# Performance work log

Hardware: AMD Instinct MI355X
Metric: run time of the kernel (lower is better)

Reference implementation:

```python
import jax, jax.numpy as jnp
import numpy as np

N, E, D, C = 40000, 640000, 128, 64


def setup_inputs() -> dict:
    key = jax.random.key(0)
    ks = jax.random.split(key, 12)
    x = jax.random.normal(ks[0], (N, D), dtype=jnp.float32)
    edge_row = jax.random.randint(ks[1], (E,), 0, N, dtype=jnp.int32)
    edge_col = jax.random.randint(ks[2], (E,), 0, N, dtype=jnp.int32)
    edge_val = jax.random.uniform(ks[3], (E,), dtype=jnp.float32)
    s1 = 1.0 / np.sqrt(D)
    W1 = jax.random.uniform(ks[4], (D, D), minval=-s1, maxval=s1, dtype=jnp.float32)
    b1 = jax.random.uniform(ks[5], (D,), minval=-s1, maxval=s1, dtype=jnp.float32)
    W2 = jax.random.uniform(ks[6], (D, D), minval=-s1, maxval=s1, dtype=jnp.float32)
    b2 = jax.random.uniform(ks[7], (D,), minval=-s1, maxval=s1, dtype=jnp.float32)
    Wf = jax.random.uniform(ks[8], (D, C), minval=-s1, maxval=s1, dtype=jnp.float32)
    bf = jax.random.uniform(ks[9], (C,), minval=-s1, maxval=s1, dtype=jnp.float32)
    return {"x": x, "edge_row": edge_row, "edge_col": edge_col, "edge_val": edge_val,
            "W1": W1, "b1": b1, "W2": W2, "b2": b2, "Wf": Wf, "bf": bf}


def _spmm(row, col, val, dense):
    # out[row] += val * dense[col]  == adj @ dense with adj in COO form
    msgs = dense[col] * val[:, None]  # [E, D]
    return jax.ops.segment_sum(msgs, row, num_segments=N)


def reference(x, edge_row, edge_col, edge_val, W1, b1, W2, b2, Wf, bf):
    # gc1: relu(adj @ (x @ W1) + b1)
    h = jax.nn.relu(_spmm(edge_row, edge_col, edge_val, x @ W1) + b1)
    # dropout(p=0.2, training=False) -> identity in eval mode
    # gc2 + residual: relu(adj @ (h @ W2) + b2) + h
    h2 = jax.nn.relu(_spmm(edge_row, edge_col, edge_val, h @ W2) + b2) + h
    # final linear classifier
    return h2 @ Wf + bf
```

## Files before the change

kernel.cpp:

```cpp
#include <hip/hip_runtime.h>

#define N_NODES 40000
#define N_EDGES 640000
#define DIM     128
#define NCLS    64
#define CAP     64
#define CSTRIDE 16

typedef __attribute__((ext_vector_type(8))) short short8v;
typedef __attribute__((ext_vector_type(4))) float f32x4;

__device__ __forceinline__ unsigned short f2bf(float f) {
    unsigned int u = __float_as_uint(f);
    unsigned int r = u + 0x7fffu + ((u >> 16) & 1u);
    return (unsigned short)(r >> 16);
}
__device__ __forceinline__ float bf2f(unsigned int s) {
    return __uint_as_float(s << 16);
}
__device__ __forceinline__ float4 dec4(uint2 u) {
    return make_float4(bf2f(u.x & 0xffffu), bf2f(u.x >> 16),
                       bf2f(u.y & 0xffffu), bf2f(u.y >> 16));
}

__launch_bounds__(256)
__global__ void prep(const float* __restrict__ W1, const float* __restrict__ W2,
                     const float* __restrict__ Wf,
                     unsigned short* __restrict__ wt1, unsigned short* __restrict__ wt2,
                     unsigned short* __restrict__ wtf, int* __restrict__ counts) {
    const int b = blockIdx.x, tid = threadIdx.x;
    if (b < 2500) {
        counts[b * 256 + tid] = 0;
    } else if (b < 2564) {
        int e = (b - 2500) * 256 + tid;
        int k = e >> 7, n = e & 127;
        wt1[n * 128 + k] = f2bf(W1[e]);
    } else if (b < 2628) {
        int e = (b - 2564) * 256 + tid;
        int k = e >> 7, n = e & 127;
        wt2[n * 128 + k] = f2bf(W2[e]);
    } else {
        int e = (b - 2628) * 256 + tid;
        int k = e >> 6, n = e & 63;
        wtf[n * 128 + k] = f2bf(Wf[e]);
    }
}

__launch_bounds__(256)
__global__ void build_bucket(const int* __restrict__ erow, const int* __restrict__ ecol,
                             const float* __restrict__ evalv, int* __restrict__ counts,
                             uint2* __restrict__ bslot) {
    int e = blockIdx.x * blockDim.x + threadIdx.x;
    if (e >= N_EDGES) return;
    int r = erow[e];
    int p = atomicAdd(&counts[r * CSTRIDE], 1);
    if (p < CAP)
        bslot[(size_t)r * CAP + p] = make_uint2((unsigned)ecol[e], __float_as_uint(evalv[e]));
}

__launch_bounds__(256)
__global__ void gemm_f32A_bf16(const float* __restrict__ A,
                               const unsigned short* __restrict__ WT,
                               unsigned short* __restrict__ C) {
    __shared__ unsigned short sB[128 * 128];
    const int tid = threadIdx.x;
    for (int c = tid; c < 2048; c += 256) {
        int n = c >> 4, j = c & 15;
        short8v v = *reinterpret_cast<const short8v*>(WT + n * 128 + 8 * j);
        *reinterpret_cast<short8v*>(&sB[n * 128 + 8 * (j ^ (n & 7))]) = v;
    }
    __syncthreads();

    const int lane = tid & 63;
    const int wv   = tid >> 6;
    const int m0   = blockIdx.x * 64 + wv * 16;
    const int r    = lane & 15;
    const int g    = lane >> 4;

    short8v af[4];
    const float* arow = A + (size_t)(m0 + r) * 128 + 8 * g;
#pragma unroll
    for (int f = 0; f < 4; ++f) {
        float4 p = *reinterpret_cast<const float4*>(arow + 32 * f);
        float4 q = *reinterpret_cast<const float4*>(arow + 32 * f + 4);
        short8v a;
        a[0] = (short)f2bf(p.x); a[1] = (short)f2bf(p.y);
        a[2] = (short)f2bf(p.z); a[3] = (short)f2bf(p.w);
        a[4] = (short)f2bf(q.x); a[5] = (short)f2bf(q.y);
        a[6] = (short)f2bf(q.z); a[7] = (short)f2bf(q.w);
        af[f] = a;
    }

    f32x4 acc[8];
#pragma unroll
    for (int nt = 0; nt < 8; ++nt) acc[nt] = (f32x4){0.f, 0.f, 0.f, 0.f};

#pragma unroll
    for (int nt = 0; nt < 8; ++nt) {
        const int rw = nt * 16 + r;
        const unsigned short* bbase = &sB[rw * 128];
#pragma unroll
        for (int f = 0; f < 4; ++f) {
            short8v bfr = *reinterpret_cast<const short8v*>(bbase + 8 * ((4 * f + g) ^ (rw & 7)));
            acc[nt] = __builtin_amdgcn_mfma_f32_16x16x32_bf16(af[f], bfr, acc[nt], 0, 0, 0);
        }
    }
#pragma unroll
    for (int nt = 0; nt < 8; ++nt)
#pragma unroll
        for (int rr = 0; rr < 4; ++rr)
            C[(size_t)(m0 + g * 4 + rr) * 128 + nt * 16 + r] = f2bf(acc[nt][rr]);
}

__launch_bounds__(256)
__global__ void gemm_bf16_128(const unsigned short* __restrict__ A,
                              const unsigned short* __restrict__ WT,
                              unsigned short* __restrict__ C) {
    __shared__ unsigned short sB[128 * 128];
    const int tid = threadIdx.x;
    for (int c = tid; c < 2048; c += 256) {
        int n = c >> 4, j = c & 15;
        short8v v = *reinterpret_cast<const short8v*>(WT + n * 128 + 8 * j);
        *reinterpret_cast<short8v*>(&sB[n * 128 + 8 * (j ^ (n & 7))]) = v;
    }
    __syncthreads();

    const int lane = tid & 63;
    const int wv   = tid >> 6;
    const int m0   = blockIdx.x * 64 + wv * 16;
    const int r    = lane & 15;
    const int g    = lane >> 4;

    short8v af[4];
    const unsigned short* arow = A + (size_t)(m0 + r) * 128 + 8 * g;
#pragma unroll
    for (int f = 0; f < 4; ++f)
        af[f] = *reinterpret_cast<const short8v*>(arow + 32 * f);

    f32x4 acc[8];
#pragma unroll
    for (int nt = 0; nt < 8; ++nt) acc[nt] = (f32x4){0.f, 0.f, 0.f, 0.f};

#pragma unroll
    for (int nt = 0; nt < 8; ++nt) {
        const int rw = nt * 16 + r;
        const unsigned short* bbase = &sB[rw * 128];
#pragma unroll
        for (int f = 0; f < 4; ++f) {
            short8v bfr = *reinterpret_cast<const short8v*>(bbase + 8 * ((4 * f + g) ^ (rw & 7)));
            acc[nt] = __builtin_amdgcn_mfma_f32_16x16x32_bf16(af[f], bfr, acc[nt], 0, 0, 0);
        }
    }
#pragma unroll
    for (int nt = 0; nt < 8; ++nt)
#pragma unroll
        for (int rr = 0; rr < 4; ++rr)
            C[(size_t)(m0 + g * 4 + rr) * 128 + nt * 16 + r] = f2bf(acc[nt][rr]);
}

__launch_bounds__(256)
__global__ void gemm_bf16_final(const unsigned short* __restrict__ A,
                                const unsigned short* __restrict__ WT,
                                const float* __restrict__ bias,
                                float* __restrict__ C) {
    __shared__ unsigned short sB[64 * 128];
    const int tid = threadIdx.x;
    for (int c = tid; c < 1024; c += 256) {
        int n = c >> 4, j = c & 15;
        short8v v = *reinterpret_cast<const short8v*>(WT + n * 128 + 8 * j);
        *reinterpret_cast<short8v*>(&sB[n * 128 + 8 * (j ^ (n & 7))]) = v;
    }
    __syncthreads();

    const int lane = tid & 63;
    const int wv   = tid >> 6;
    const int m0   = blockIdx.x * 64 + wv * 16;
    const int r    = lane & 15;
    const int g    = lane >> 4;

    short8v af[4];
    const unsigned short* arow = A + (size_t)(m0 + r) * 128 + 8 * g;
#pragma unroll
    for (int f = 0; f < 4; ++f)
        af[f] = *reinterpret_cast<const short8v*>(arow + 32 * f);

    f32x4 acc[4];
#pragma unroll
    for (int nt = 0; nt < 4; ++nt) acc[nt] = (f32x4){0.f, 0.f, 0.f, 0.f};

#pragma unroll
    for (int nt = 0; nt < 4; ++nt) {
        const int rw = nt * 16 + r;
        const unsigned short* bbase = &sB[rw * 128];
#pragma unroll
        for (int f = 0; f < 4; ++f) {
            short8v bfr = *reinterpret_cast<const short8v*>(bbase + 8 * ((4 * f + g) ^ (rw & 7)));
            acc[nt] = __builtin_amdgcn_mfma_f32_16x16x32_bf16(af[f], bfr, acc[nt], 0, 0, 0);
        }
    }
#pragma unroll
    for (int nt = 0; nt < 4; ++nt)
#pragma unroll
        for (int rr = 0; rr < 4; ++rr)
            C[(size_t)(m0 + g * 4 + rr) * 64 + nt * 16 + r] = acc[nt][rr] + bias[nt * 16 + r];
}

__launch_bounds__(256)
__global__ void spmm_fused_bf16(const uint2* __restrict__ dense2,
                                const uint2* __restrict__ bslot,
                                const int* __restrict__ counts,
                                const float4* __restrict__ bias4,
                                const uint2* __restrict__ residbf,
                                uint2* __restrict__ outbf) {
    const int lane = threadIdx.x & 63;
    const int half = lane >> 5;
    const int sub  = lane & 31;
    const int row  = blockIdx.x * 4 + (threadIdx.x >> 6);
    int deg = counts[row * CSTRIDE];
    if (deg > CAP) deg = CAP;

    int   colr = 0;
    float valr = 0.f;
    if (lane < deg) {
        uint2 s = bslot[(size_t)row * CAP + lane];
        colr = (int)s.x;
        valr = __uint_as_float(s.y);
    }
    const int degUp = (deg + 7) & ~7;

    float ax0 = 0.f, ay0 = 0.f, az0 = 0.f, aw0 = 0.f;
    float ax1 = 0.f, ay1 = 0.f, az1 = 0.f, aw1 = 0.f;
    float ax2 = 0.f, ay2 = 0.f, az2 = 0.f, aw2 = 0.f;
    float ax3 = 0.f, ay3 = 0.f, az3 = 0.f, aw3 = 0.f;
    for (int i = 0; i < degUp; i += 8) {
        int   c0 = __shfl(colr, i + 0 + half); float v0 = __shfl(valr, i + 0 + half);
        int   c1 = __shfl(colr, i + 2 + half); float v1 = __shfl(valr, i + 2 + half);
        int   c2 = __shfl(colr, i + 4 + half); float v2 = __shfl(valr, i + 4 + half);
        int   c3 = __shfl(colr, i + 6 + half); float v3 = __shfl(valr, i + 6 + half);
        uint2 u0 = dense2[(size_t)c0 * 32 + sub];
        uint2 u1 = dense2[(size_t)c1 * 32 + sub];
        uint2 u2 = dense2[(size_t)c2 * 32 + sub];
        uint2 u3 = dense2[(size_t)c3 * 32 + sub];
        float4 d0 = dec4(u0); ax0 += v0 * d0.x; ay0 += v0 * d0.y; az0 += v0 * d0.z; aw0 += v0 * d0.w;
        float4 d1 = dec4(u1); ax1 += v1 * d1.x; ay1 += v1 * d1.y; az1 += v1 * d1.z; aw1 += v1 * d1.w;
        float4 d2 = dec4(u2); ax2 += v2 * d2.x; ay2 += v2 * d2.y; az2 += v2 * d2.z; aw2 += v2 * d2.w;
        float4 d3 = dec4(u3); ax3 += v3 * d3.x; ay3 += v3 * d3.y; az3 += v3 * d3.z; aw3 += v3 * d3.w;
    }
    float sx = (ax0 + ax1) + (ax2 + ax3);
    float sy = (ay0 + ay1) + (ay2 + ay3);
    float sz = (az0 + az1) + (az2 + az3);
    float sw = (aw0 + aw1) + (aw2 + aw3);
    sx += __shfl_xor(sx, 32);
    sy += __shfl_xor(sy, 32);
    sz += __shfl_xor(sz, 32);
    sw += __shfl_xor(sw, 32);

    if (half == 0) {
        float4 bb = bias4[sub];
        sx = fmaxf(sx + bb.x, 0.f);
        sy = fmaxf(sy + bb.y, 0.f);
        sz = fmaxf(sz + bb.z, 0.f);
        sw = fmaxf(sw + bb.w, 0.f);
        if (residbf) {
            float4 rr = dec4(residbf[(size_t)row * 32 + sub]);
            sx += rr.x; sy += rr.y; sz += rr.z; sw += rr.w;
        }
        outbf[(size_t)row * 32 + sub] =
            make_uint2((unsigned)f2bf(sx) | ((unsigned)f2bf(sy) << 16),
                       (unsigned)f2bf(sz) | ((unsigned)f2bf(sw) << 16));
    }
}

extern "C" void kernel_launch(void* const* d_in, const int* in_sizes, int n_in,
                              void* d_out, int out_size, void* d_ws, size_t ws_size,
                              hipStream_t stream) {
    const float* x    = (const float*)d_in[0];
    const int*   erow = (const int*)  d_in[1];
    const int*   ecol = (const int*)  d_in[2];
    const float* ev   = (const float*)d_in[3];
    const float* W1   = (const float*)d_in[4];
    const float* b1   = (const float*)d_in[5];
    const float* W2   = (const float*)d_in[6];
    const float* b2   = (const float*)d_in[7];
    const float* Wf   = (const float*)d_in[8];
    const float* bf   = (const float*)d_in[9];
    float* out = (float*)d_out;

    const size_t MB = 1u << 20;
    char* ws = (char*)d_ws;
    int*            counts = (int*)           (ws + 0 * MB);
    uint2*          bslot  = (uint2*)         (ws + 4 * MB);
    unsigned short* gb     = (unsigned short*)(ws + 25 * MB);
    unsigned short* hb     = (unsigned short*)(ws + 36 * MB);
    unsigned short* h2b    = (unsigned short*)(ws + 47 * MB);
    unsigned short* wt1    = (unsigned short*)(ws + 58 * MB);
    unsigned short* wt2    = (unsigned short*)(ws + 58 * MB + 65536);
    unsigned short* wtf    = (unsigned short*)(ws + 58 * MB + 131072);

    prep<<<2660, 256, 0, stream>>>(W1, W2, Wf, wt1, wt2, wtf, counts);
    build_bucket<<<(N_EDGES + 255) / 256, 256, 0, stream>>>(erow, ecol, ev, counts, bslot);

    gemm_f32A_bf16<<<N_NODES / 64, 256, 0, stream>>>(x, wt1, gb);
    spmm_fused_bf16<<<N_NODES / 4, 256, 0, stream>>>((const uint2*)gb, bslot, counts,
                                                     (const float4*)b1, nullptr,
                                                     (uint2*)hb);
    gemm_bf16_128<<<N_NODES / 64, 256, 0, stream>>>(hb, wt2, gb);
    spmm_fused_bf16<<<N_NODES / 4, 256, 0, stream>>>((const uint2*)gb, bslot, counts,
                                                     (const float4*)b2, (const uint2*)hb,
                                                     (uint2*)h2b);
    gemm_bf16_final<<<N_NODES / 64, 256, 0, stream>>>(h2b, wtf, bf, out);
}
```

Baseline: 188.0 us.

## Fuse final classifier GEMM into second SpMM and vectorize edge bucketing

Folds the final linear layer into the second SpMM kernel: each block stages Wf in shared memory as fp32 and computes the 64 outputs per row with scalar FMAs. This removes the h2 intermediate write/read and one kernel launch. Edge bucketing now reads four edges per thread with vector loads. The trade-off is that every 4-row block reloads the full 32KB Wf into LDS, which adds heavy L2 traffic, lowers occupancy, and replaces MFMA with scalar fp32 math.

```diff
diff --git a/kernel.cpp b/kernel.cpp
--- a/kernel.cpp
+++ b/kernel.cpp
@@ -25,9 +25,8 @@
 
 __launch_bounds__(256)
 __global__ void prep(const float* __restrict__ W1, const float* __restrict__ W2,
-                     const float* __restrict__ Wf,
                      unsigned short* __restrict__ wt1, unsigned short* __restrict__ wt2,
-                     unsigned short* __restrict__ wtf, int* __restrict__ counts) {
+                     int* __restrict__ counts) {
     const int b = blockIdx.x, tid = threadIdx.x;
     if (b < 2500) {
         counts[b * 256 + tid] = 0;
@@ -35,27 +34,29 @@
         int e = (b - 2500) * 256 + tid;
         int k = e >> 7, n = e & 127;
         wt1[n * 128 + k] = f2bf(W1[e]);
-    } else if (b < 2628) {
+    } else {
         int e = (b - 2564) * 256 + tid;
         int k = e >> 7, n = e & 127;
         wt2[n * 128 + k] = f2bf(W2[e]);
-    } else {
-        int e = (b - 2628) * 256 + tid;
-        int k = e >> 6, n = e & 63;
-        wtf[n * 128 + k] = f2bf(Wf[e]);
-    }
-}
-
-__launch_bounds__(256)
-__global__ void build_bucket(const int* __restrict__ erow, const int* __restrict__ ecol,
-                             const float* __restrict__ evalv, int* __restrict__ counts,
+    }
+}
+
+__launch_bounds__(256)
+__global__ void build_bucket(const int4* __restrict__ erow4, const int4* __restrict__ ecol4,
+                             const float4* __restrict__ ev4, int* __restrict__ counts,
                              uint2* __restrict__ bslot) {
-    int e = blockIdx.x * blockDim.x + threadIdx.x;
-    if (e >= N_EDGES) return;
-    int r = erow[e];
-    int p = atomicAdd(&counts[r * CSTRIDE], 1);
-    if (p < CAP)
-        bslot[(size_t)r * CAP + p] = make_uint2((unsigned)ecol[e], __float_as_uint(evalv[e]));
+    int t = blockIdx.x * 256 + threadIdx.x;
+    int4   r = erow4[t];
+    int4   c = ecol4[t];
+    float4 v = ev4[t];
+    int p0 = atomicAdd(&counts[r.x * CSTRIDE], 1);
+    int p1 = atomicAdd(&counts[r.y * CSTRIDE], 1);
+    int p2 = atomicAdd(&counts[r.z * CSTRIDE], 1);
+    int p3 = atomicAdd(&counts[r.w * CSTRIDE], 1);
+    if (p0 < CAP) bslot[(size_t)r.x * CAP + p0] = make_uint2((unsigned)c.x, __float_as_uint(v.x));
+    if (p1 < CAP) bslot[(size_t)r.y * CAP + p1] = make_uint2((unsigned)c.y, __float_as_uint(v.y));
+    if (p2 < CAP) bslot[(size_t)r.z * CAP + p2] = make_uint2((unsigned)c.z, __float_as_uint(v.z));
+    if (p3 < CAP) bslot[(size_t)r.w * CAP + p3] = make_uint2((unsigned)c.w, __float_as_uint(v.w));
 }
 
 __launch_bounds__(256)
@@ -159,58 +160,10 @@
 }
 
 __launch_bounds__(256)
-__global__ void gemm_bf16_final(const unsigned short* __restrict__ A,
-                                const unsigned short* __restrict__ WT,
-                                const float* __restrict__ bias,
-                                float* __restrict__ C) {
-    __shared__ unsigned short sB[64 * 128];
-    const int tid = threadIdx.x;
-    for (int c = tid; c < 1024; c += 256) {
-        int n = c >> 4, j = c & 15;
-        short8v v = *reinterpret_cast<const short8v*>(WT + n * 128 + 8 * j);
-        *reinterpret_cast<short8v*>(&sB[n * 128 + 8 * (j ^ (n & 7))]) = v;
-    }
-    __syncthreads();
-
-    const int lane = tid & 63;
-    const int wv   = tid >> 6;
-    const int m0   = blockIdx.x * 64 + wv * 16;
-    const int r    = lane & 15;
-    const int g    = lane >> 4;
-
-    short8v af[4];
-    const unsigned short* arow = A + (size_t)(m0 + r) * 128 + 8 * g;
-#pragma unroll
-    for (int f = 0; f < 4; ++f)
-        af[f] = *reinterpret_cast<const short8v*>(arow + 32 * f);
-
-    f32x4 acc[4];
-#pragma unroll
-    for (int nt = 0; nt < 4; ++nt) acc[nt] = (f32x4){0.f, 0.f, 0.f, 0.f};
-
-#pragma unroll
-    for (int nt = 0; nt < 4; ++nt) {
-        const int rw = nt * 16 + r;
-        const unsigned short* bbase = &sB[rw * 128];
-#pragma unroll
-        for (int f = 0; f < 4; ++f) {
-            short8v bfr = *reinterpret_cast<const short8v*>(bbase + 8 * ((4 * f + g) ^ (rw & 7)));
-            acc[nt] = __builtin_amdgcn_mfma_f32_16x16x32_bf16(af[f], bfr, acc[nt], 0, 0, 0);
-        }
-    }
-#pragma unroll
-    for (int nt = 0; nt < 4; ++nt)
-#pragma unroll
-        for (int rr = 0; rr < 4; ++rr)
-            C[(size_t)(m0 + g * 4 + rr) * 64 + nt * 16 + r] = acc[nt][rr] + bias[nt * 16 + r];
-}
-
-__launch_bounds__(256)
 __global__ void spmm_fused_bf16(const uint2* __restrict__ dense2,
                                 const uint2* __restrict__ bslot,
                                 const int* __restrict__ counts,
                                 const float4* __restrict__ bias4,
-                                const uint2* __restrict__ residbf,
                                 uint2* __restrict__ outbf) {
     const int lane = threadIdx.x & 63;
     const int half = lane >> 5;
@@ -261,14 +214,88 @@
         sy = fmaxf(sy + bb.y, 0.f);
         sz = fmaxf(sz + bb.z, 0.f);
         sw = fmaxf(sw + bb.w, 0.f);
-        if (residbf) {
-            float4 rr = dec4(residbf[(size_t)row * 32 + sub]);
-            sx += rr.x; sy += rr.y; sz += rr.z; sw += rr.w;
-        }
         outbf[(size_t)row * 32 + sub] =
             make_uint2((unsigned)f2bf(sx) | ((unsigned)f2bf(sy) << 16),
                        (unsigned)f2bf(sz) | ((unsigned)f2bf(sw) << 16));
     }
+}
+
+__launch_bounds__(256)
+__global__ void spmm_final_fused(const uint2* __restrict__ dense2,
+                                 const uint2* __restrict__ bslot,
+                                 const int* __restrict__ counts,
+                                 const float4* __restrict__ bias4,
+                                 const uint2* __restrict__ residbf,
+                                 const float4* __restrict__ Wf4,
+                                 const float* __restrict__ bf,
+                                 float* __restrict__ out) {
+    __shared__ float sWf[128 * 64];
+    __shared__ float sH[4][128];
+    const int tid  = threadIdx.x;
+#pragma unroll
+    for (int i = tid; i < 2048; i += 256)
+        *reinterpret_cast<float4*>(&sWf[i * 4]) = Wf4[i];
+
+    const int lane = tid & 63;
+    const int half = lane >> 5;
+    const int sub  = lane & 31;
+    const int rl   = tid >> 6;
+    const int row  = blockIdx.x * 4 + rl;
+    int deg = counts[row * CSTRIDE];
+    if (deg > CAP) deg = CAP;
+
+    int   colr = 0;
+    float valr = 0.f;
+    if (lane < deg) {
+        uint2 s = bslot[(size_t)row * CAP + lane];
+        colr = (int)s.x;
+        valr = __uint_as_float(s.y);
+    }
+    const int degUp = (deg + 7) & ~7;
+
+    float ax0 = 0.f, ay0 = 0.f, az0 = 0.f, aw0 = 0.f;
+    float ax1 = 0.f, ay1 = 0.f, az1 = 0.f, aw1 = 0.f;
+    float ax2 = 0.f, ay2 = 0.f, az2 = 0.f, aw2 = 0.f;
+    float ax3 = 0.f, ay3 = 0.f, az3 = 0.f, aw3 = 0.f;
+    for (int i = 0; i < degUp; i += 8) {
+        int   c0 = __shfl(colr, i + 0 + half); float v0 = __shfl(valr, i + 0 + half);
+        int   c1 = __shfl(colr, i + 2 + half); float v1 = __shfl(valr, i + 2 + half);
+        int   c2 = __shfl(colr, i + 4 + half); float v2 = __shfl(valr, i + 4 + half);
+        int   c3 = __shfl(colr, i + 6 + half); float v3 = __shfl(valr, i + 6 + half);
+        uint2 u0 = dense2[(size_t)c0 * 32 + sub];
+        uint2 u1 = dense2[(size_t)c1 * 32 + sub];
+        uint2 u2 = dense2[(size_t)c2 * 32 + sub];
+        uint2 u3 = dense2[(size_t)c3 * 32 + sub];
+        float4 d0 = dec4(u0); ax0 += v0 * d0.x; ay0 += v0 * d0.y; az0 += v0 * d0.z; aw0 += v0 * d0.w;
+        float4 d1 = dec4(u1); ax1 += v1 * d1.x; ay1 += v1 * d1.y; az1 += v1 * d1.z; aw1 += v1 * d1.w;
+        float4 d2 = dec4(u2); ax2 += v2 * d2.x; ay2 += v2 * d2.y; az2 += v2 * d2.z; aw2 += v2 * d2.w;
+        float4 d3 = dec4(u3); ax3 += v3 * d3.x; ay3 += v3 * d3.y; az3 += v3 * d3.z; aw3 += v3 * d3.w;
+    }
+    float sx = (ax0 + ax1) + (ax2 + ax3);
+    float sy = (ay0 + ay1) + (ay2 + ay3);
+    float sz = (az0 + az1) + (az2 + az3);
+    float sw = (aw0 + aw1) + (aw2 + aw3);
+    sx += __shfl_xor(sx, 32);
+    sy += __shfl_xor(sy, 32);
+    sz += __shfl_xor(sz, 32);
+    sw += __shfl_xor(sw, 32);
+
+    if (half == 0) {
+        float4 bb = bias4[sub];
+        float4 rr = dec4(residbf[(size_t)row * 32 + sub]);
+        sH[rl][4 * sub + 0] = fmaxf(sx + bb.x, 0.f) + rr.x;
+        sH[rl][4 * sub + 1] = fmaxf(sy + bb.y, 0.f) + rr.y;
+        sH[rl][4 * sub + 2] = fmaxf(sz + bb.z, 0.f) + rr.z;
+        sH[rl][4 * sub + 3] = fmaxf(sw + bb.w, 0.f) + rr.w;
+    }
+    __syncthreads();
+
+    const int col = lane;
+    float acc = bf[col];
+#pragma unroll 16
+    for (int k = 0; k < 128; ++k)
+        acc += sH[rl][k] * sWf[k * 64 + col];
+    out[(size_t)row * 64 + col] = acc;
 }
 
 extern "C" void kernel_launch(void* const* d_in, const int* in_sizes, int n_in,
@@ -292,21 +319,18 @@
     uint2*          bslot  = (uint2*)         (ws + 4 * MB);
     unsigned short* gb     = (unsigned short*)(ws + 25 * MB);
     unsigned short* hb     = (unsigned short*)(ws + 36 * MB);
-    unsigned short* h2b    = (unsigned short*)(ws + 47 * MB);
-    unsigned short* wt1    = (unsigned short*)(ws + 58 * MB);
-    unsigned short* wt2    = (unsigned short*)(ws + 58 * MB + 65536);
-    unsigned short* wtf    = (unsigned short*)(ws + 58 * MB + 131072);
-
-    prep<<<2660, 256, 0, stream>>>(W1, W2, Wf, wt1, wt2, wtf, counts);
-    build_bucket<<<(N_EDGES + 255) / 256, 256, 0, stream>>>(erow, ecol, ev, counts, bslot);
+    unsigned short* wt1    = (unsigned short*)(ws + 47 * MB);
+    unsigned short* wt2    = (unsigned short*)(ws + 47 * MB + 65536);
+
+    prep<<<2628, 256, 0, stream>>>(W1, W2, wt1, wt2, counts);
+    build_bucket<<<N_EDGES / 4 / 256, 256, 0, stream>>>(
+        (const int4*)erow, (const int4*)ecol, (const float4*)ev, counts, bslot);
 
     gemm_f32A_bf16<<<N_NODES / 64, 256, 0, stream>>>(x, wt1, gb);
     spmm_fused_bf16<<<N_NODES / 4, 256, 0, stream>>>((const uint2*)gb, bslot, counts,
-                                                     (const float4*)b1, nullptr,
-                                                     (uint2*)hb);
+                                                     (const float4*)b1, (uint2*)hb);
     gemm_bf16_128<<<N_NODES / 64, 256, 0, stream>>>(hb, wt2, gb);
-    spmm_fused_bf16<<<N_NODES / 4, 256, 0, stream>>>((const uint2*)gb, bslot, counts,
-                                                     (const float4*)b2, (const uint2*)hb,
-                                                     (uint2*)h2b);
-    gemm_bf16_final<<<N_NODES / 64, 256, 0, stream>>>(h2b, wtf, bf, out);
-}
+    spmm_final_fused<<<N_NODES / 4, 256, 0, stream>>>((const uint2*)gb, bslot, counts,
+                                                      (const float4*)b2, (const uint2*)hb,
+                                                      (const float4*)Wf, bf, out);
+}
```

Result: slower. 222.6 us (+18.4%).
